# Performance work log

Measured on AMD Instinct MI355X. Metric: run time of the kernel, lower is better.

Reference implementation:

```python
import jax, jax.numpy as jnp
import numpy as np

DIM = 1024
HEADS = 16
HEAD_DIM = DIM // HEADS
WINDOW = 512
NEG = -1e9  # matches masked_fill(-1e9) semantics; excluded keys get ~0 weight


def setup_inputs() -> dict:
    key = jax.random.key(0)
    ks = jax.random.split(key, 9)
    s = 1.0 / np.sqrt(DIM)
    inp = {"x": jax.random.normal(ks[0], (2, 4096, DIM), dtype=jnp.float32)}
    for i, name in enumerate(["q", "k", "v", "o"]):
        inp[f"W{name}"] = jax.random.uniform(ks[1 + 2 * i], (DIM, DIM), jnp.float32, -s, s)
        inp[f"b{name}"] = jax.random.uniform(ks[2 + 2 * i], (DIM,), jnp.float32, -s, s)
    return inp


def _sliding_window_attn(x, Wq, bq, Wk, bk, Wv, bv, Wo, bo):
    B, S, D = x.shape
    H, hd, W = HEADS, HEAD_DIM, WINDOW
    nb = S // W  # number of query blocks

    def proj(Wp, bp):
        y = x @ Wp.T + bp                       # [B,S,D]
        return y.reshape(B, S, H, hd).transpose(0, 2, 1, 3)  # [B,H,S,hd]

    q = proj(Wq, bq)
    k = proj(Wk, bk)
    v = proj(Wv, bv)

    scale = hd ** -0.5
    qb = q.reshape(B, H, nb, W, hd)

    def window_kv(t):
        # each query block n attends to blocks n-1 and n (2W keys)
        pad = jnp.concatenate([jnp.zeros((B, H, W, hd), t.dtype), t], axis=2)
        prev = pad[:, :, :S].reshape(B, H, nb, W, hd)
        cur = t.reshape(B, H, nb, W, hd)
        return jnp.concatenate([prev, cur], axis=3)  # [B,H,nb,2W,hd]

    kw = window_kv(k)
    vw = window_kv(v)

    scores = jnp.einsum('bhnqd,bhnkd->bhnqk', qb, kw) * scale  # [B,H,nb,W,2W]

    # key abs pos = n*W - W + t ; query abs pos = n*W + s
    t = jnp.arange(2 * W)            # [2W]
    s_ = jnp.arange(W)[:, None]      # [W,1]
    n = jnp.arange(nb)[:, None, None]  # [nb,1,1]
    valid = (t <= s_ + W) & (t >= s_ + 1) & (n * W - W + t >= 0)  # [nb,W,2W]
    scores = jnp.where(valid, scores, NEG)

    attn = jax.nn.softmax(scores, axis=-1)
    out = jnp.einsum('bhnqk,bhnkd->bhnqd', attn, vw)  # [B,H,nb,W,hd]
    out = out.reshape(B, H, S, hd).transpose(0, 2, 1, 3).reshape(B, S, D)
    return out @ Wo.T + bo


def reference(x, Wq, bq, Wk, bk, Wv, bv, Wo, bo):
    return _sliding_window_attn(x, Wq, bq, Wk, bk, Wv, bv, Wo, bo)
```

## Files before the change

### kernel.cpp

```cpp
#include <hip/hip_runtime.h>
#include <hip/hip_bf16.h>

typedef __bf16 bf16_t;
typedef __attribute__((ext_vector_type(8))) __bf16 bfrag;
typedef __attribute__((ext_vector_type(4))) __bf16 bf16x4;
typedef __attribute__((ext_vector_type(4))) float f32x4;

#define SEQ    4096
#define NDIM   1024
#define NHEAD  16
#define HD     64
#define NBATCH 2
#define MROWS  (NBATCH * SEQ)
#define LQK    2048
#define PSTR   76

__device__ __forceinline__ void gload_lds16(const bf16_t* g, bf16_t* l) {
    __builtin_amdgcn_global_load_lds(
        (const __attribute__((address_space(1))) unsigned int*)g,
        (__attribute__((address_space(3))) unsigned int*)l,
        16, 0, 0);
}

template <typename OT>
__global__ __launch_bounds__(256, 2)
void gemm_bt(const bf16_t* __restrict__ A, int lda,
             const bf16_t* __restrict__ W,
             const float* __restrict__ b0p, const float* __restrict__ b1p,
             const float* __restrict__ b2p,
             OT* __restrict__ C, int ldc, int K,
             bf16_t* __restrict__ VtOut)
{
    __shared__ __align__(16) bf16_t As[128 * 32];
    __shared__ __align__(16) bf16_t Bs[128 * 32];

    const int tid  = threadIdx.x;
    const int lane = tid & 63;
    const int wid  = tid >> 6;
    const int n16  = lane & 15;
    const int quad = lane >> 4;
    const int row0 = blockIdx.y * 128;
    const int col0 = blockIdx.x * 128;
    const int wrow = (wid >> 1) * 64;
    const int wcol = (wid & 1) * 64;
    const float* bias = (col0 < 1024) ? b0p : (col0 < 2048 ? b1p : b2p);
    const int bcol0 = col0 & 1023;

    f32x4 acc[4][4];
#pragma unroll
    for (int i = 0; i < 4; i++)
#pragma unroll
        for (int j = 0; j < 4; j++) acc[i][j] = (f32x4){0.f, 0.f, 0.f, 0.f};

    for (int k0 = 0; k0 < K; k0 += 32) {
#pragma unroll
        for (int it = 0; it < 2; it++) {
            int idx = tid + it * 256;
            int r   = idx >> 2;
            int c   = (idx & 3) * 8;
            gload_lds16(A + (size_t)(row0 + r) * lda + k0 + c, &As[(it * 256 + wid * 64) * 8]);
            gload_lds16(W + (size_t)(col0 + r) * K   + k0 + c, &Bs[(it * 256 + wid * 64) * 8]);
        }
        __syncthreads();

        bfrag af[4], bfg[4];
#pragma unroll
        for (int i = 0; i < 4; i++)
            af[i] = *(const bfrag*)(&As[(wrow + i * 16 + n16) * 32 + quad * 8]);
#pragma unroll
        for (int j = 0; j < 4; j++)
            bfg[j] = *(const bfrag*)(&Bs[(wcol + j * 16 + n16) * 32 + quad * 8]);

#pragma unroll
        for (int i = 0; i < 4; i++)
#pragma unroll
            for (int j = 0; j < 4; j++)
                acc[i][j] = __builtin_amdgcn_mfma_f32_16x16x32_bf16(af[i], bfg[j], acc[i][j], 0, 0, 0);
        __syncthreads();
    }

    if (col0 < 2048 || VtOut == nullptr) {
#pragma unroll
        for (int i = 0; i < 4; i++)
#pragma unroll
            for (int j = 0; j < 4; j++)
#pragma unroll
                for (int r = 0; r < 4; r++) {
                    int row = row0 + wrow + i * 16 + quad * 4 + r;
                    int col = wcol + j * 16 + n16;
                    float v = acc[i][j][r] + bias[bcol0 + col];
                    C[(size_t)row * ldc + col0 + col] = (OT)v;
                }
    } else {
#pragma unroll
        for (int i = 0; i < 4; i++) {
#pragma unroll
            for (int j = 0; j < 4; j++) {
                int dg     = col0 + wcol + j * 16 + n16 - 2048;
                int token0 = row0 + wrow + i * 16 + quad * 4;
                int bb     = token0 >> 12;
                float bv   = bias[bcol0 + wcol + j * 16 + n16];
                size_t vrow = ((size_t)bb * NHEAD + (dg >> 6)) * HD + (dg & 63);
                bf16x4 pk;
#pragma unroll
                for (int r = 0; r < 4; r++) pk[r] = (__bf16)(acc[i][j][r] + bv);
                *(bf16x4*)&VtOut[vrow * SEQ + (token0 & (SEQ - 1))] = pk;
            }
        }
    }
}

__global__ __launch_bounds__(256)
void cast_x(const float* __restrict__ s, bf16_t* __restrict__ d)
{
    size_t i = ((size_t)blockIdx.x * 256 + threadIdx.x) * 8;
    float4 a = *(const float4*)(s + i);
    float4 b = *(const float4*)(s + i + 4);
    bfrag o;
    o[0] = (__bf16)a.x; o[1] = (__bf16)a.y; o[2] = (__bf16)a.z; o[3] = (__bf16)a.w;
    o[4] = (__bf16)b.x; o[5] = (__bf16)b.y; o[6] = (__bf16)b.z; o[7] = (__bf16)b.w;
    *(bfrag*)(d + i) = o;
}

__global__ __launch_bounds__(256)
void cast_w(const float* __restrict__ wq, const float* __restrict__ wk,
            const float* __restrict__ wv, const float* __restrict__ wo,
            bf16_t* __restrict__ d)
{
    size_t t   = (size_t)blockIdx.x * 256 + threadIdx.x;
    int    sel = (int)(t >> 17);
    const float* s = sel == 0 ? wq : (sel == 1 ? wk : (sel == 2 ? wv : wo));
    size_t off = (t & 131071) * 8;
    float4 a = *(const float4*)(s + off);
    float4 b = *(const float4*)(s + off + 4);
    bfrag o;
    o[0] = (__bf16)a.x; o[1] = (__bf16)a.y; o[2] = (__bf16)a.z; o[3] = (__bf16)a.w;
    o[4] = (__bf16)b.x; o[5] = (__bf16)b.y; o[6] = (__bf16)b.z; o[7] = (__bf16)b.w;
    *(bfrag*)(d + (size_t)sel * 1048576 + off) = o;
}

__global__ __launch_bounds__(256, 4)
void attn_win(const bf16_t* __restrict__ QK, const bf16_t* __restrict__ Vt,
              bf16_t* __restrict__ AO)
{
    __shared__ __align__(16) bf16_t Ks[2][64 * 72];
    __shared__ __align__(16) bf16_t Pw[4][16 * PSTR];

    const int tid  = threadIdx.x;
    const int wid  = tid >> 6;
    const int lane = tid & 63;
    const int n16  = lane & 15;
    const int quad = lane >> 4;

    const int q0 = blockIdx.x * 64;
    const int bh = blockIdx.y;
    const int b  = bh >> 4, h = bh & 15;
    const size_t bS   = (size_t)b * SEQ;
    const size_t hoff = (size_t)h * HD;
    const bf16_t* Vb  = Vt + (size_t)bh * HD * SEQ;
    const int wstart  = q0 - 512;
    const int it0     = (q0 < 512) ? ((512 - q0) >> 6) : 0;

    const int srow  = tid >> 2;
    const int scol0 = (tid & 3) * 16;

    const int qa = q0 + wid * 16 + n16;
    bfrag bq0 = *(const bfrag*)(&QK[(bS + qa) * LQK + hoff + quad * 8]);
    bfrag bq1 = *(const bfrag*)(&QK[(bS + qa) * LQK + hoff + 32 + quad * 8]);

    f32x4 ao[4];
#pragma unroll
    for (int j = 0; j < 4; j++) ao[j] = (f32x4){0.f, 0.f, 0.f, 0.f};
    float m = -1e30f, l = 0.f;

    uint4 kp0, kp1;
    {
        const bf16_t* src = &QK[(bS + wstart + it0 * 64 + srow) * LQK + 1024 + hoff + scol0];
        kp0 = *(const uint4*)(src);
        kp1 = *(const uint4*)(src + 8);
    }

    for (int it = it0; it < 9; ++it) {
        const int k0 = wstart + it * 64;
        const int pb = it & 1;
        *(uint4*)(&Ks[pb][srow * 72 + scol0])     = kp0;
        *(uint4*)(&Ks[pb][srow * 72 + scol0 + 8]) = kp1;
        __syncthreads();
        if (it < 8) {
            const bf16_t* src = &QK[(bS + wstart + (it + 1) * 64 + srow) * LQK + 1024 + hoff + scol0];
            kp0 = *(const uint4*)(src);
            kp1 = *(const uint4*)(src + 8);
        }

        f32x4 a[4];
#pragma unroll
        for (int nt = 0; nt < 4; nt++) {
            bfrag ak0 = *(const bfrag*)(&Ks[pb][(nt * 16 + n16) * 72 + quad * 8]);
            bfrag ak1 = *(const bfrag*)(&Ks[pb][(nt * 16 + n16) * 72 + 32 + quad * 8]);
            f32x4 s4 = (f32x4){0.f, 0.f, 0.f, 0.f};
            s4 = __builtin_amdgcn_mfma_f32_16x16x32_bf16(ak0, bq0, s4, 0, 0, 0);
            s4 = __builtin_amdgcn_mfma_f32_16x16x32_bf16(ak1, bq1, s4, 0, 0, 0);
            a[nt] = s4;
        }

        const bool msk = (it == 0) || (it == 8);
        if (msk) {
#pragma unroll
            for (int nt = 0; nt < 4; nt++)
#pragma unroll
                for (int r = 0; r < 4; r++) {
                    int ka = k0 + nt * 16 + quad * 4 + r;
                    bool valid = (ka >= qa - 511) & (ka <= qa);
                    a[nt][r] = valid ? a[nt][r] * 0.125f : -1e30f;
                }
        } else {
#pragma unroll
            for (int nt = 0; nt < 4; nt++)
#pragma unroll
                for (int r = 0; r < 4; r++) a[nt][r] *= 0.125f;
        }

        float cm = -1e30f;
#pragma unroll
        for (int nt = 0; nt < 4; nt++)
#pragma unroll
            for (int r = 0; r < 4; r++) cm = fmaxf(cm, a[nt][r]);
        cm = fmaxf(cm, __shfl_xor(cm, 16, 64));
        cm = fmaxf(cm, __shfl_xor(cm, 32, 64));
        float mn    = fmaxf(m, cm);
        float alpha = __expf(m - mn);
        m = mn;
#pragma unroll
        for (int j = 0; j < 4; j++)
#pragma unroll
            for (int r = 0; r < 4; r++) ao[j][r] *= alpha;

        float lacc = 0.f;
#pragma unroll
        for (int nt = 0; nt < 4; nt++) {
            bf16x4 pk;
#pragma unroll
            for (int r = 0; r < 4; r++) {
                float p = __expf(a[nt][r] - m);
                if (msk && a[nt][r] <= -1e29f) p = 0.f;
                lacc += p;
                pk[r] = (__bf16)p;
            }
            *(bf16x4*)&Pw[wid][n16 * PSTR + nt * 16 + quad * 4] = pk;
        }
        l = l * alpha + lacc;

#pragma unroll
        for (int ks = 0; ks < 2; ks++) {
            bfrag bp = *(const bfrag*)(&Pw[wid][n16 * PSTR + ks * 32 + quad * 8]);
#pragma unroll
            for (int j = 0; j < 4; j++) {
                bfrag av = *(const bfrag*)(&Vb[(size_t)(j * 16 + n16) * SEQ
                                               + k0 + ks * 32 + quad * 8]);
                ao[j] = __builtin_amdgcn_mfma_f32_16x16x32_bf16(av, bp, ao[j], 0, 0, 0);
            }
        }
    }

    l += __shfl_xor(l, 16, 64);
    l += __shfl_xor(l, 32, 64);
    const float inv = 1.0f / l;
#pragma unroll
    for (int j = 0; j < 4; j++) {
        bf16x4 pk;
#pragma unroll
        for (int r = 0; r < 4; r++) pk[r] = (__bf16)(ao[j][r] * inv);
        *(bf16x4*)&AO[(bS + qa) * NDIM + hoff + j * 16 + quad * 4] = pk;
    }
}

extern "C" void kernel_launch(void* const* d_in, const int* in_sizes, int n_in,
                              void* d_out, int out_size, void* d_ws, size_t ws_size,
                              hipStream_t stream)
{
    const float* x  = (const float*)d_in[0];
    const float* Wq = (const float*)d_in[1];
    const float* bq = (const float*)d_in[2];
    const float* Wk = (const float*)d_in[3];
    const float* bk = (const float*)d_in[4];
    const float* Wv = (const float*)d_in[5];
    const float* bv = (const float*)d_in[6];
    const float* Wo = (const float*)d_in[7];
    const float* bo = (const float*)d_in[8];
    float* out = (float*)d_out;

    const size_t QK_E = (size_t)MROWS * LQK;
    const size_t X_E  = (size_t)MROWS * NDIM;
    if (ws_size < (QK_E + X_E + 4u * 1048576u) * sizeof(bf16_t)) return;

    bf16_t* QKb = (bf16_t*)d_ws;
    bf16_t* AbX = QKb + QK_E;
    bf16_t* Wc  = AbX + X_E;
    bf16_t* Wob = Wc + 3u * 1048576u;
    bf16_t* Vtg = (bf16_t*)d_out;

    dim3 blk(256);

    cast_x<<<dim3(4096), blk, 0, stream>>>(x, AbX);
    cast_w<<<dim3(2048), blk, 0, stream>>>(Wq, Wk, Wv, Wo, Wc);

    gemm_bt<bf16_t><<<dim3(3072 / 128, MROWS / 128), blk, 0, stream>>>(
        AbX, NDIM, Wc, bq, bk, bv, QKb, LQK, NDIM, Vtg);

    attn_win<<<dim3(SEQ / 64, NBATCH * NHEAD), blk, 0, stream>>>(QKb, Vtg, AbX);

    gemm_bt<float><<<dim3(NDIM / 128, MROWS / 128), blk, 0, stream>>>(
        AbX, NDIM, Wob, bo, bo, bo, out, NDIM, NDIM, nullptr);
}
```

Baseline: 279.3 us.

## Enlarge attention query tile to 128, fold softmax scale into Wq

The attention kernel now processes 128 queries per block, with each wave handling two 16-query groups. Each staged K tile and each V fragment load is therefore reused across twice as many queries, and waves skip K tiles that fall outside their window. The 1/sqrt(hd) scale is folded into the bf16 Wq cast and the q bias, which removes the per-score multiply. The grid is linearized and remapped across batch-head and query tiles, and the kernel gains one extra K iteration per block. In exchange the kernel uses more registers and has fewer blocks, and the earlier bf16 rounding of the scaled Wq changes numerics slightly.

```diff
diff --git a/kernel.cpp b/kernel.cpp
--- a/kernel.cpp
+++ b/kernel.cpp
@@ -27,7 +27,7 @@
 void gemm_bt(const bf16_t* __restrict__ A, int lda,
              const bf16_t* __restrict__ W,
              const float* __restrict__ b0p, const float* __restrict__ b1p,
-             const float* __restrict__ b2p,
+             const float* __restrict__ b2p, float qscale,
              OT* __restrict__ C, int ldc, int K,
              bf16_t* __restrict__ VtOut)
 {
@@ -44,6 +44,7 @@
     const int wrow = (wid >> 1) * 64;
     const int wcol = (wid & 1) * 64;
     const float* bias = (col0 < 1024) ? b0p : (col0 < 2048 ? b1p : b2p);
+    const float bsc = (col0 < 1024) ? qscale : 1.0f;
     const int bcol0 = col0 & 1023;
 
     f32x4 acc[4][4];
@@ -88,7 +89,7 @@
                 for (int r = 0; r < 4; r++) {
                     int row = row0 + wrow + i * 16 + quad * 4 + r;
                     int col = wcol + j * 16 + n16;
-                    float v = acc[i][j][r] + bias[bcol0 + col];
+                    float v = acc[i][j][r] + bias[bcol0 + col] * bsc;
                     C[(size_t)row * ldc + col0 + col] = (OT)v;
                 }
     } else {
@@ -130,12 +131,15 @@
     size_t t   = (size_t)blockIdx.x * 256 + threadIdx.x;
     int    sel = (int)(t >> 17);
     const float* s = sel == 0 ? wq : (sel == 1 ? wk : (sel == 2 ? wv : wo));
+    const float sc = (sel == 0) ? 0.125f : 1.0f;
     size_t off = (t & 131071) * 8;
     float4 a = *(const float4*)(s + off);
     float4 b = *(const float4*)(s + off + 4);
     bfrag o;
-    o[0] = (__bf16)a.x; o[1] = (__bf16)a.y; o[2] = (__bf16)a.z; o[3] = (__bf16)a.w;
-    o[4] = (__bf16)b.x; o[5] = (__bf16)b.y; o[6] = (__bf16)b.z; o[7] = (__bf16)b.w;
+    o[0] = (__bf16)(a.x * sc); o[1] = (__bf16)(a.y * sc);
+    o[2] = (__bf16)(a.z * sc); o[3] = (__bf16)(a.w * sc);
+    o[4] = (__bf16)(b.x * sc); o[5] = (__bf16)(b.y * sc);
+    o[6] = (__bf16)(b.z * sc); o[7] = (__bf16)(b.w * sc);
     *(bfrag*)(d + (size_t)sel * 1048576 + off) = o;
 }
 
@@ -144,7 +148,7 @@
               bf16_t* __restrict__ AO)
 {
     __shared__ __align__(16) bf16_t Ks[2][64 * 72];
-    __shared__ __align__(16) bf16_t Pw[4][16 * PSTR];
+    __shared__ __align__(16) bf16_t Pw[4][32 * PSTR];
 
     const int tid  = threadIdx.x;
     const int wid  = tid >> 6;
@@ -152,26 +156,39 @@
     const int n16  = lane & 15;
     const int quad = lane >> 4;
 
-    const int q0 = blockIdx.x * 64;
-    const int bh = blockIdx.y;
+    const int lin = blockIdx.x;
+    const int sub = lin >> 3;
+    const int bh  = (lin & 7) * 4 + (sub >> 5);
+    const int qt  = sub & 31;
+    const int qb0 = qt * 128;
+
     const int b  = bh >> 4, h = bh & 15;
     const size_t bS   = (size_t)b * SEQ;
     const size_t hoff = (size_t)h * HD;
     const bf16_t* Vb  = Vt + (size_t)bh * HD * SEQ;
-    const int wstart  = q0 - 512;
-    const int it0     = (q0 < 512) ? ((512 - q0) >> 6) : 0;
+    const int wstart  = qb0 - 512;
+    const int it0     = (qb0 < 512) ? ((512 - qb0) >> 6) : 0;
 
     const int srow  = tid >> 2;
     const int scol0 = (tid & 3) * 16;
 
-    const int qa = q0 + wid * 16 + n16;
-    bfrag bq0 = *(const bfrag*)(&QK[(bS + qa) * LQK + hoff + quad * 8]);
-    bfrag bq1 = *(const bfrag*)(&QK[(bS + qa) * LQK + hoff + 32 + quad * 8]);
-
-    f32x4 ao[4];
-#pragma unroll
-    for (int j = 0; j < 4; j++) ao[j] = (f32x4){0.f, 0.f, 0.f, 0.f};
-    float m = -1e30f, l = 0.f;
+    const int qwmin = qb0 + wid * 32;
+    const int qwmax = qwmin + 31;
+    int qa[2];
+    bfrag bq0[2], bq1[2];
+#pragma unroll
+    for (int qg = 0; qg < 2; qg++) {
+        qa[qg] = qwmin + qg * 16 + n16;
+        bq0[qg] = *(const bfrag*)(&QK[(bS + qa[qg]) * LQK + hoff + quad * 8]);
+        bq1[qg] = *(const bfrag*)(&QK[(bS + qa[qg]) * LQK + hoff + 32 + quad * 8]);
+    }
+
+    f32x4 ao[2][4];
+#pragma unroll
+    for (int qg = 0; qg < 2; qg++)
+#pragma unroll
+        for (int j = 0; j < 4; j++) ao[qg][j] = (f32x4){0.f, 0.f, 0.f, 0.f};
+    float m[2] = {-1e30f, -1e30f}, l[2] = {0.f, 0.f};
 
     uint4 kp0, kp1;
     {
@@ -180,97 +197,109 @@
         kp1 = *(const uint4*)(src + 8);
     }
 
-    for (int it = it0; it < 9; ++it) {
+    for (int it = it0; it < 10; ++it) {
         const int k0 = wstart + it * 64;
         const int pb = it & 1;
         *(uint4*)(&Ks[pb][srow * 72 + scol0])     = kp0;
         *(uint4*)(&Ks[pb][srow * 72 + scol0 + 8]) = kp1;
         __syncthreads();
-        if (it < 8) {
+        if (it < 9) {
             const bf16_t* src = &QK[(bS + wstart + (it + 1) * 64 + srow) * LQK + 1024 + hoff + scol0];
             kp0 = *(const uint4*)(src);
             kp1 = *(const uint4*)(src + 8);
         }
 
-        f32x4 a[4];
+        if (k0 > qwmax || k0 + 63 < qwmin - 511) continue;
+
+        f32x4 a[2][4];
 #pragma unroll
         for (int nt = 0; nt < 4; nt++) {
             bfrag ak0 = *(const bfrag*)(&Ks[pb][(nt * 16 + n16) * 72 + quad * 8]);
             bfrag ak1 = *(const bfrag*)(&Ks[pb][(nt * 16 + n16) * 72 + 32 + quad * 8]);
-            f32x4 s4 = (f32x4){0.f, 0.f, 0.f, 0.f};
-            s4 = __builtin_amdgcn_mfma_f32_16x16x32_bf16(ak0, bq0, s4, 0, 0, 0);
-            s4 = __builtin_amdgcn_mfma_f32_16x16x32_bf16(ak1, bq1, s4, 0, 0, 0);
-            a[nt] = s4;
-        }
-
-        const bool msk = (it == 0) || (it == 8);
-        if (msk) {
+#pragma unroll
+            for (int qg = 0; qg < 2; qg++) {
+                f32x4 s4 = (f32x4){0.f, 0.f, 0.f, 0.f};
+                s4 = __builtin_amdgcn_mfma_f32_16x16x32_bf16(ak0, bq0[qg], s4, 0, 0, 0);
+                s4 = __builtin_amdgcn_mfma_f32_16x16x32_bf16(ak1, bq1[qg], s4, 0, 0, 0);
+                a[qg][nt] = s4;
+            }
+        }
+
+#pragma unroll
+        for (int qg = 0; qg < 2; qg++) {
+            const int gmin = qwmin + qg * 16, gmax = gmin + 15;
+            const bool msk = !((k0 >= gmax - 511) & (k0 + 63 <= gmin));
+            if (msk) {
+#pragma unroll
+                for (int nt = 0; nt < 4; nt++)
+#pragma unroll
+                    for (int r = 0; r < 4; r++) {
+                        int ka = k0 + nt * 16 + quad * 4 + r;
+                        bool valid = (ka >= qa[qg] - 511) & (ka <= qa[qg]);
+                        if (!valid) a[qg][nt][r] = -1e30f;
+                    }
+            }
+
+            float cm = -1e30f;
 #pragma unroll
             for (int nt = 0; nt < 4; nt++)
 #pragma unroll
+                for (int r = 0; r < 4; r++) cm = fmaxf(cm, a[qg][nt][r]);
+            cm = fmaxf(cm, __shfl_xor(cm, 16, 64));
+            cm = fmaxf(cm, __shfl_xor(cm, 32, 64));
+            float mn    = fmaxf(m[qg], cm);
+            float alpha = __expf(m[qg] - mn);
+            m[qg] = mn;
+#pragma unroll
+            for (int j = 0; j < 4; j++)
+#pragma unroll
+                for (int r = 0; r < 4; r++) ao[qg][j][r] *= alpha;
+
+            float lacc = 0.f;
+#pragma unroll
+            for (int nt = 0; nt < 4; nt++) {
+                bf16x4 pk;
+#pragma unroll
                 for (int r = 0; r < 4; r++) {
-                    int ka = k0 + nt * 16 + quad * 4 + r;
-                    bool valid = (ka >= qa - 511) & (ka <= qa);
-                    a[nt][r] = valid ? a[nt][r] * 0.125f : -1e30f;
+                    float p = __expf(a[qg][nt][r] - m[qg]);
+                    lacc += p;
+                    pk[r] = (__bf16)p;
                 }
-        } else {
-#pragma unroll
-            for (int nt = 0; nt < 4; nt++)
-#pragma unroll
-                for (int r = 0; r < 4; r++) a[nt][r] *= 0.125f;
-        }
-
-        float cm = -1e30f;
-#pragma unroll
-        for (int nt = 0; nt < 4; nt++)
-#pragma unroll
-            for (int r = 0; r < 4; r++) cm = fmaxf(cm, a[nt][r]);
-        cm = fmaxf(cm, __shfl_xor(cm, 16, 64));
-        cm = fmaxf(cm, __shfl_xor(cm, 32, 64));
-        float mn    = fmaxf(m, cm);
-        float alpha = __expf(m - mn);
-        m = mn;
-#pragma unroll
-        for (int j = 0; j < 4; j++)
-#pragma unroll
-            for (int r = 0; r < 4; r++) ao[j][r] *= alpha;
-
-        float lacc = 0.f;
-#pragma unroll
-        for (int nt = 0; nt < 4; nt++) {
-            bf16x4 pk;
-#pragma unroll
-            for (int r = 0; r < 4; r++) {
-                float p = __expf(a[nt][r] - m);
-                if (msk && a[nt][r] <= -1e29f) p = 0.f;
-                lacc += p;
-                pk[r] = (__bf16)p;
-            }
-            *(bf16x4*)&Pw[wid][n16 * PSTR + nt * 16 + quad * 4] = pk;
-        }
-        l = l * alpha + lacc;
+                *(bf16x4*)&Pw[wid][(qg * 16 + n16) * PSTR + nt * 16 + quad * 4] = pk;
+            }
+            l[qg] = l[qg] * alpha + lacc;
+        }
 
 #pragma unroll
         for (int ks = 0; ks < 2; ks++) {
-            bfrag bp = *(const bfrag*)(&Pw[wid][n16 * PSTR + ks * 32 + quad * 8]);
+            bfrag bp[2];
+#pragma unroll
+            for (int qg = 0; qg < 2; qg++)
+                bp[qg] = *(const bfrag*)(&Pw[wid][(qg * 16 + n16) * PSTR + ks * 32 + quad * 8]);
 #pragma unroll
             for (int j = 0; j < 4; j++) {
                 bfrag av = *(const bfrag*)(&Vb[(size_t)(j * 16 + n16) * SEQ
                                                + k0 + ks * 32 + quad * 8]);
-                ao[j] = __builtin_amdgcn_mfma_f32_16x16x32_bf16(av, bp, ao[j], 0, 0, 0);
-            }
-        }
-    }
-
-    l += __shfl_xor(l, 16, 64);
-    l += __shfl_xor(l, 32, 64);
-    const float inv = 1.0f / l;
-#pragma unroll
-    for (int j = 0; j < 4; j++) {
-        bf16x4 pk;
-#pragma unroll
-        for (int r = 0; r < 4; r++) pk[r] = (__bf16)(ao[j][r] * inv);
-        *(bf16x4*)&AO[(bS + qa) * NDIM + hoff + j * 16 + quad * 4] = pk;
+#pragma unroll
+                for (int qg = 0; qg < 2; qg++)
+                    ao[qg][j] = __builtin_amdgcn_mfma_f32_16x16x32_bf16(av, bp[qg], ao[qg][j], 0, 0, 0);
+            }
+        }
+    }
+
+#pragma unroll
+    for (int qg = 0; qg < 2; qg++) {
+        float lv = l[qg];
+        lv += __shfl_xor(lv, 16, 64);
+        lv += __shfl_xor(lv, 32, 64);
+        const float inv = 1.0f / lv;
+#pragma unroll
+        for (int j = 0; j < 4; j++) {
+            bf16x4 pk;
+#pragma unroll
+            for (int r = 0; r < 4; r++) pk[r] = (__bf16)(ao[qg][j][r] * inv);
+            *(bf16x4*)&AO[(bS + qa[qg]) * NDIM + hoff + j * 16 + quad * 4] = pk;
+        }
     }
 }
 
@@ -305,10 +334,10 @@
     cast_w<<<dim3(2048), blk, 0, stream>>>(Wq, Wk, Wv, Wo, Wc);
 
     gemm_bt<bf16_t><<<dim3(3072 / 128, MROWS / 128), blk, 0, stream>>>(
-        AbX, NDIM, Wc, bq, bk, bv, QKb, LQK, NDIM, Vtg);
-
-    attn_win<<<dim3(SEQ / 64, NBATCH * NHEAD), blk, 0, stream>>>(QKb, Vtg, AbX);
+        AbX, NDIM, Wc, bq, bk, bv, 0.125f, QKb, LQK, NDIM, Vtg);
+
+    attn_win<<<dim3(1024), dim3(256), 0, stream>>>(QKb, Vtg, AbX);
 
     gemm_bt<float><<<dim3(NDIM / 128, MROWS / 128), blk, 0, stream>>>(
-        AbX, NDIM, Wob, bo, bo, bo, out, NDIM, NDIM, nullptr);
-}
+        AbX, NDIM, Wob, bo, bo, bo, 1.0f, out, NDIM, NDIM, nullptr);
+}
```

Measured after the change: 271.0 us. 1.03x faster.
